# Optimization experiments

Hardware: AMD Instinct MI355X
Metric: run time of the kernel (lower is better)

The kernel has to match this reference:

```python
import jax, jax.numpy as jnp
import numpy as np

N_NODES = 50000
N_EDGES = 800000
HIDDEN = 128


def setup_inputs() -> dict:
    key = jax.random.key(0)
    k_h, k_src, k_dst, k_w1, k_w2 = jax.random.split(key, 5)
    h = jax.random.normal(k_h, (N_NODES, HIDDEN), dtype=jnp.float32)
    src = jax.random.randint(k_src, (N_EDGES,), 0, N_NODES, dtype=jnp.int32)
    dst = jax.random.randint(k_dst, (N_EDGES,), 0, N_NODES, dtype=jnp.int32)
    edge_index = jnp.stack([src, dst], axis=0)
    # MLP params (torch Linear: y = x @ W.T + b); store as [in, out] for einsum
    s1 = 1.0 / np.sqrt(2 * HIDDEN)
    s2 = 1.0 / np.sqrt(HIDDEN)
    W1 = jax.random.uniform(k_w1, (2 * HIDDEN, HIDDEN), jnp.float32, -s1, s1)
    b1 = jnp.zeros((HIDDEN,), jnp.float32)
    W2 = jax.random.uniform(k_w2, (HIDDEN, HIDDEN), jnp.float32, -s2, s2)
    b2 = jnp.zeros((HIDDEN,), jnp.float32)
    return {"h": h, "edge_index": edge_index, "W1": W1, "b1": b1, "W2": W2, "b2": b2}


def reference(h, edge_index, W1, b1, W2, b2):
    src, dst = edge_index[0], edge_index[1]
    n = h.shape[0]
    # scatter-add of gathered source features -> agg [N, H]
    agg = jax.ops.segment_sum(h[src], dst, num_segments=n)
    # degree normalization (clamp_min 1)
    deg = jax.ops.segment_sum(jnp.ones_like(dst, dtype=h.dtype), dst, num_segments=n)
    deg = jnp.maximum(deg, 1.0)[:, None]
    agg = agg / deg
    x = jnp.concatenate([h, agg], axis=1)  # [N, 2H]
    x = jax.nn.relu(x @ W1 + b1)
    x = jax.nn.relu(x @ W2 + b2)
    return x
```

## Files before the change

kernel.cpp:

```cpp
#include <hip/hip_runtime.h>

typedef unsigned short u16;
typedef unsigned int u32;
typedef __attribute__((ext_vector_type(8))) short short8;
typedef __attribute__((ext_vector_type(4))) float f32x4;
typedef __attribute__((ext_vector_type(4))) u32 u32x4;

#define BKT_SHIFT 7
#define BKT_NODES 128
#define CAP 3072
#define EPB 4096

__device__ inline u16 f2bf(float f){ u32 u=__float_as_uint(f); u32 r=((u>>16)&1u)+0x7fffu; return (u16)((u+r)>>16); }

__global__ __launch_bounds__(256) void k_cast(
    const float* __restrict__ h, u32* __restrict__ outw, int nh8,
    const float* __restrict__ w1, const float* __restrict__ w2,
    u16* __restrict__ w1t, u16* __restrict__ w2t,
    int* __restrict__ gcnt, int nbuck){
  int e = blockIdx.x*256 + threadIdx.x;
  if (e < nh8){
    float4 a = *(const float4*)(h + (size_t)e*8);
    float4 b = *(const float4*)(h + (size_t)e*8 + 4);
    u32x4 p;
    p.x = (u32)f2bf(a.x) | ((u32)f2bf(a.y)<<16);
    p.y = (u32)f2bf(a.z) | ((u32)f2bf(a.w)<<16);
    p.z = (u32)f2bf(b.x) | ((u32)f2bf(b.y)<<16);
    p.w = (u32)f2bf(b.z) | ((u32)f2bf(b.w)<<16);
    int node = e>>4, c8 = e&15;
    *(u32x4*)(outw + (size_t)node*128 + c8*4) = p;
  }
  if (e < 256*128){ int k=e>>7, nn=e&127; w1t[nn*256+k]=f2bf(w1[e]); }
  else { int j=e-256*128; if (j<128*128){ int k=j>>7, nn=j&127; w2t[nn*128+k]=f2bf(w2[j]); } }
  if (e < nbuck) gcnt[e] = 0;
}

__global__ __launch_bounds__(256) void k_bin(
    const int* __restrict__ src, const int* __restrict__ dst,
    int* __restrict__ gcnt, u32* __restrict__ recs_g, int nE){
  __shared__ u32 rl[EPB];
  __shared__ int hist[512];
  __shared__ int curs[512];
  int t = threadIdx.x;
  int e0 = blockIdx.x*EPB;
  for (int i=t;i<512;i+=256) hist[i]=0;
  __syncthreads();
  #pragma unroll
  for (int i=0;i<EPB/256;i++){
    int e = e0 + i*256 + t;
    u32 rec = 0xffffffffu;
    if (e < nE){
      u32 d = (u32)dst[e];
      u32 s = (u32)src[e];
      u32 b = d >> BKT_SHIFT;
      rec = (b<<23) | ((d & (u32)(BKT_NODES-1))<<16) | s;
      atomicAdd(&hist[b], 1);
    }
    rl[i*256+t] = rec;
  }
  __syncthreads();
  for (int i=t;i<512;i+=256){
    int c = hist[i];
    curs[i] = c ? atomicAdd(&gcnt[i], c) : 0;
  }
  __syncthreads();
  #pragma unroll
  for (int i=0;i<EPB/256;i++){
    u32 rec = rl[i*256+t];
    if (rec != 0xffffffffu){
      u32 b = rec>>23;
      int slot = atomicAdd(&curs[b], 1);
      if (slot < CAP) recs_g[(size_t)b*CAP + slot] = rec & 0x7fffffu;
    }
  }
}

__global__ __launch_bounds__(512) void k_agg2(
    const u32* __restrict__ recs_g, const int* __restrict__ gcnt,
    u32* __restrict__ outw, int n){
  __shared__ u32 stage[CAP];
  __shared__ u16 srt[CAP];
  __shared__ int hist[BKT_NODES];
  __shared__ int scn[BKT_NODES];
  __shared__ int cur[BKT_NODES];
  int b = blockIdx.x, t = threadIdx.x;
  int cnt = gcnt[b]; if (cnt > CAP) cnt = CAP;
  if (t < BKT_NODES) hist[t] = 0;
  __syncthreads();
  for (int i=t; i<cnt; i+=512){
    u32 r = recs_g[(size_t)b*CAP + i];
    stage[i] = r;
    atomicAdd(&hist[(r>>16)&(BKT_NODES-1)], 1);
  }
  __syncthreads();
  if (t < BKT_NODES) scn[t] = hist[t];
  __syncthreads();
  #pragma unroll
  for (int d=1; d<BKT_NODES; d<<=1){
    int v = 0;
    if (t < BKT_NODES){ v = scn[t]; if (t >= d) v += scn[t-d]; }
    __syncthreads();
    if (t < BKT_NODES) scn[t] = v;
    __syncthreads();
  }
  if (t < BKT_NODES) cur[t] = scn[t] - hist[t];
  __syncthreads();
  for (int i=t; i<cnt; i+=512){
    u32 r = stage[i];
    int slot = atomicAdd(&cur[(r>>16)&(BKT_NODES-1)], 1);
    srt[slot] = (u16)(r & 0xffffu);
  }
  __syncthreads();
  int wave = t>>6, lane = t&63;
  for (int nl=wave; nl<BKT_NODES; nl+=8){
    int node = b*BKT_NODES + nl;
    if (node >= n) continue;
    int deg = hist[nl];
    int st  = scn[nl] - deg;
    float a0=0.f, a1=0.f;
    int nfull = deg >> 4;
    for (int bb=0; bb<nfull; bb++){
      int base = st + bb*16;
      int sidx[16];
      #pragma unroll
      for (int j=0;j<16;j++) sidx[j] = srt[base+j];
      u32 vv[16];
      #pragma unroll
      for (int j=0;j<16;j++) vv[j] = outw[(size_t)sidx[j]*128 + lane];
      #pragma unroll
      for (int j=0;j<16;j++){
        union{u32 u; float f;} lo,hi; lo.u=vv[j]<<16; hi.u=vv[j]&0xffff0000u;
        a0 += lo.f; a1 += hi.f;
      }
    }
    int rem = deg & 15;
    if (rem){
      int base = st + nfull*16;
      int sidx[16];
      #pragma unroll
      for (int j=0;j<16;j++) sidx[j] = srt[base + (j<rem ? j : rem-1)];
      u32 vv[16];
      #pragma unroll
      for (int j=0;j<16;j++) vv[j] = outw[(size_t)sidx[j]*128 + lane];
      #pragma unroll
      for (int j=0;j<16;j++){
        float m = (j<rem) ? 1.f : 0.f;
        union{u32 u; float f;} lo,hi; lo.u=vv[j]<<16; hi.u=vv[j]&0xffff0000u;
        a0 += m*lo.f; a1 += m*hi.f;
      }
    }
    float inv = 1.f/(float)(deg>0?deg:1);
    outw[(size_t)node*128 + 64 + lane] = (u32)f2bf(a0*inv) | ((u32)f2bf(a1*inv)<<16);
  }
}

__global__ __launch_bounds__(256, 4) void k_mlp(
    const u32* __restrict__ outw_in,
    const u16* __restrict__ w1t, const u16* __restrict__ w2t,
    const float* __restrict__ b1, const float* __restrict__ b2,
    float* __restrict__ out, int n){
  __shared__ __align__(16) u16 xs[64*264];
  int t = threadIdx.x;
  int node0 = blockIdx.x*64;
  int wave=t>>6, lane=t&63, quad=lane>>4, l16=lane&15;
  int nt0 = wave*2;

  const u16* w1p0 = w1t + (size_t)((nt0  )*16 + l16)*256 + quad*8;
  const u16* w1p1 = w1t + (size_t)((nt0+1)*16 + l16)*256 + quad*8;
  short8 wb1[16];
  #pragma unroll
  for (int ks=0;ks<8;ks++){
    wb1[ks*2+0] = *(const short8*)(w1p0 + ks*32);
    wb1[ks*2+1] = *(const short8*)(w1p1 + ks*32);
  }

  #pragma unroll
  for (int i=0;i<8;i++){
    int idx = i*256 + t;
    int row = idx>>5, c8 = idx&31;
    int node = node0 + row;
    u32x4 v = {0,0,0,0};
    if (node < n) v = *(const u32x4*)(outw_in + (size_t)node*128 + c8*4);
    *(u32x4*)(&xs[row*264 + c8*8]) = v;
  }
  __syncthreads();

  f32x4 acc[4][2];
  #pragma unroll
  for (int m=0;m<4;m++){ acc[m][0]=(f32x4){0,0,0,0}; acc[m][1]=(f32x4){0,0,0,0}; }
  #pragma unroll
  for (int ks=0;ks<8;ks++){
    #pragma unroll
    for (int m=0;m<4;m++){
      short8 a = *(const short8*)(&xs[(m*16+l16)*264 + ks*32 + quad*8]);
      acc[m][0] = __builtin_amdgcn_mfma_f32_16x16x32_bf16(a, wb1[ks*2+0], acc[m][0],0,0,0);
      acc[m][1] = __builtin_amdgcn_mfma_f32_16x16x32_bf16(a, wb1[ks*2+1], acc[m][1],0,0,0);
    }
  }

  const u16* w2p0 = w2t + (size_t)((nt0  )*16 + l16)*128 + quad*8;
  const u16* w2p1 = w2t + (size_t)((nt0+1)*16 + l16)*128 + quad*8;
  short8 wb2[8];
  #pragma unroll
  for (int ks=0;ks<4;ks++){
    wb2[ks*2+0] = *(const short8*)(w2p0 + ks*32);
    wb2[ks*2+1] = *(const short8*)(w2p1 + ks*32);
  }

  __syncthreads();

  float bias0 = b1[(nt0  )*16 + l16];
  float bias1 = b1[(nt0+1)*16 + l16];
  #pragma unroll
  for (int m=0;m<4;m++){
    #pragma unroll
    for (int r=0;r<4;r++){
      int row = m*16 + quad*4 + r;
      float v0 = acc[m][0][r] + bias0; v0 = v0>0.f ? v0 : 0.f;
      float v1 = acc[m][1][r] + bias1; v1 = v1>0.f ? v1 : 0.f;
      xs[row*264 + (nt0  )*16 + l16] = f2bf(v0);
      xs[row*264 + (nt0+1)*16 + l16] = f2bf(v1);
    }
  }
  __syncthreads();

  f32x4 acc2[4][2];
  #pragma unroll
  for (int m=0;m<4;m++){ acc2[m][0]=(f32x4){0,0,0,0}; acc2[m][1]=(f32x4){0,0,0,0}; }
  #pragma unroll
  for (int ks=0;ks<4;ks++){
    #pragma unroll
    for (int m=0;m<4;m++){
      short8 a = *(const short8*)(&xs[(m*16+l16)*264 + ks*32 + quad*8]);
      acc2[m][0] = __builtin_amdgcn_mfma_f32_16x16x32_bf16(a, wb2[ks*2+0], acc2[m][0],0,0,0);
      acc2[m][1] = __builtin_amdgcn_mfma_f32_16x16x32_bf16(a, wb2[ks*2+1], acc2[m][1],0,0,0);
    }
  }
  float c0 = b2[(nt0  )*16 + l16];
  float c1 = b2[(nt0+1)*16 + l16];
  #pragma unroll
  for (int m=0;m<4;m++){
    #pragma unroll
    for (int r=0;r<4;r++){
      int node = node0 + m*16 + quad*4 + r;
      if (node<n){
        float v0 = acc2[m][0][r]+c0; v0 = v0>0.f?v0:0.f;
        float v1 = acc2[m][1][r]+c1; v1 = v1>0.f?v1:0.f;
        out[(size_t)node*128 + (nt0  )*16 + l16] = v0;
        out[(size_t)node*128 + (nt0+1)*16 + l16] = v1;
      }
    }
  }
}

extern "C" void kernel_launch(void* const* d_in, const int* in_sizes, int n_in,
                              void* d_out, int out_size, void* d_ws, size_t ws_size,
                              hipStream_t stream){
  const float* h  = (const float*)d_in[0];
  const int*   ei = (const int*)d_in[1];
  const float* W1 = (const float*)d_in[2];
  const float* b1 = (const float*)d_in[3];
  const float* W2 = (const float*)d_in[4];
  const float* b2 = (const float*)d_in[5];
  float* out = (float*)d_out;
  u32* outw  = (u32*)d_out;
  int n  = in_sizes[0] / 128;
  int nE = in_sizes[1] / 2;
  const int* srcI = ei;
  const int* dstI = ei + nE;
  int nbuck = (n + BKT_NODES - 1) >> BKT_SHIFT;

  char* ws = (char*)d_ws;
  u32* recs = (u32*)ws;
  size_t off = (size_t)nbuck*CAP*4;
  int* gcnt = (int*)(ws + off);
  off += (size_t)nbuck*4; off = (off + 15) & ~(size_t)15;
  u16* w1t = (u16*)(ws + off);
  u16* w2t = (u16*)(ws + off + 65536);

  int nh8 = n*16;
  int castN = nh8 > 49152 ? nh8 : 49152;
  k_cast<<<(castN+255)/256, 256, 0, stream>>>(h, outw, nh8, W1, W2, w1t, w2t, gcnt, nbuck);
  k_bin <<<(nE+EPB-1)/EPB, 256, 0, stream>>>(srcI, dstI, gcnt, recs, nE);
  k_agg2<<<nbuck, 512, 0, stream>>>(recs, gcnt, outw, n);
  k_mlp <<<(n+63)/64, 256, 0, stream>>>(outw, w1t, w2t, b1, b2, out, n);
}
```

Before: 157.1 us.

## Fuse cast with binning and aggregation with MLP into two kernels

Merges the bf16 cast and edge binning into one launch using disjoint block ranges. It also fuses the per-bucket aggregation with the two-layer MLP, so the aggregated features go straight to shared memory instead of a global round trip. Buckets shrink to 64 nodes to match the MLP tile, and the gather now uses 16-lane groups with 16-byte loads per node. A separate memset replaces the in-kernel counter clear. The tradeoffs are more shared memory and lower occupancy per block in the fused kernel, plus a smaller per-bucket capacity (1536) that could overflow on skewed inputs.

```diff
diff --git a/kernel.cpp b/kernel.cpp
--- a/kernel.cpp
+++ b/kernel.cpp
@@ -6,173 +6,87 @@
 typedef __attribute__((ext_vector_type(4))) float f32x4;
 typedef __attribute__((ext_vector_type(4))) u32 u32x4;
 
-#define BKT_SHIFT 7
-#define BKT_NODES 128
-#define CAP 3072
+#define BKT_SHIFT 6
+#define BKT_NODES 64
+#define CAP 1536
 #define EPB 4096
+#define NBH 1024
 
 __device__ inline u16 f2bf(float f){ u32 u=__float_as_uint(f); u32 r=((u>>16)&1u)+0x7fffu; return (u16)((u+r)>>16); }
 
-__global__ __launch_bounds__(256) void k_cast(
-    const float* __restrict__ h, u32* __restrict__ outw, int nh8,
+__global__ __launch_bounds__(256) void k_castbin(
+    const int* __restrict__ src, const int* __restrict__ dst,
+    int* __restrict__ gcnt, u32* __restrict__ recs_g, int nE, int gB,
+    const float* __restrict__ h, u16* __restrict__ hbf, int nh8,
     const float* __restrict__ w1, const float* __restrict__ w2,
-    u16* __restrict__ w1t, u16* __restrict__ w2t,
-    int* __restrict__ gcnt, int nbuck){
-  int e = blockIdx.x*256 + threadIdx.x;
-  if (e < nh8){
-    float4 a = *(const float4*)(h + (size_t)e*8);
-    float4 b = *(const float4*)(h + (size_t)e*8 + 4);
-    u32x4 p;
-    p.x = (u32)f2bf(a.x) | ((u32)f2bf(a.y)<<16);
-    p.y = (u32)f2bf(a.z) | ((u32)f2bf(a.w)<<16);
-    p.z = (u32)f2bf(b.x) | ((u32)f2bf(b.y)<<16);
-    p.w = (u32)f2bf(b.z) | ((u32)f2bf(b.w)<<16);
-    int node = e>>4, c8 = e&15;
-    *(u32x4*)(outw + (size_t)node*128 + c8*4) = p;
-  }
-  if (e < 256*128){ int k=e>>7, nn=e&127; w1t[nn*256+k]=f2bf(w1[e]); }
-  else { int j=e-256*128; if (j<128*128){ int k=j>>7, nn=j&127; w2t[nn*128+k]=f2bf(w2[j]); } }
-  if (e < nbuck) gcnt[e] = 0;
+    u16* __restrict__ w1t, u16* __restrict__ w2t){
+  __shared__ u32 rl[EPB];
+  __shared__ int hist[NBH];
+  __shared__ int curs[NBH];
+  int t = threadIdx.x;
+  if ((int)blockIdx.x < gB){
+    int e0 = blockIdx.x*EPB;
+    for (int i=t;i<NBH;i+=256) hist[i]=0;
+    __syncthreads();
+    #pragma unroll
+    for (int i=0;i<EPB/256;i++){
+      int e = e0 + i*256 + t;
+      u32 rec = 0xffffffffu;
+      if (e < nE){
+        u32 d = (u32)dst[e];
+        u32 s = (u32)src[e];
+        u32 bb = d >> BKT_SHIFT;
+        rec = (bb<<22) | ((d & (u32)(BKT_NODES-1))<<16) | s;
+        atomicAdd(&hist[bb & (NBH-1)], 1);
+      }
+      rl[i*256+t] = rec;
+    }
+    __syncthreads();
+    for (int i=t;i<NBH;i+=256){
+      int c = hist[i];
+      curs[i] = c ? atomicAdd(&gcnt[i], c) : 0;
+    }
+    __syncthreads();
+    #pragma unroll
+    for (int i=0;i<EPB/256;i++){
+      u32 rec = rl[i*256+t];
+      if (rec != 0xffffffffu){
+        u32 bb = rec>>22;
+        int slot = atomicAdd(&curs[bb], 1);
+        if (slot < CAP) recs_g[(size_t)bb*CAP + slot] = rec & 0x3fffffu;
+      }
+    }
+  } else {
+    int e = ((int)blockIdx.x - gB)*256 + t;
+    if (e < nh8){
+      float4 a = *(const float4*)(h + (size_t)e*8);
+      float4 b = *(const float4*)(h + (size_t)e*8 + 4);
+      u32x4 p;
+      p.x = (u32)f2bf(a.x) | ((u32)f2bf(a.y)<<16);
+      p.y = (u32)f2bf(a.z) | ((u32)f2bf(a.w)<<16);
+      p.z = (u32)f2bf(b.x) | ((u32)f2bf(b.y)<<16);
+      p.w = (u32)f2bf(b.z) | ((u32)f2bf(b.w)<<16);
+      *(u32x4*)(hbf + (size_t)e*8) = p;
+    }
+    if (e < 256*128){ int k=e>>7, nn=e&127; w1t[nn*256+k]=f2bf(w1[e]); }
+    else { int j=e-256*128; if (j<128*128){ int k=j>>7, nn=j&127; w2t[nn*128+k]=f2bf(w2[j]); } }
+  }
 }
 
-__global__ __launch_bounds__(256) void k_bin(
-    const int* __restrict__ src, const int* __restrict__ dst,
-    int* __restrict__ gcnt, u32* __restrict__ recs_g, int nE){
-  __shared__ u32 rl[EPB];
-  __shared__ int hist[512];
-  __shared__ int curs[512];
-  int t = threadIdx.x;
-  int e0 = blockIdx.x*EPB;
-  for (int i=t;i<512;i+=256) hist[i]=0;
-  __syncthreads();
-  #pragma unroll
-  for (int i=0;i<EPB/256;i++){
-    int e = e0 + i*256 + t;
-    u32 rec = 0xffffffffu;
-    if (e < nE){
-      u32 d = (u32)dst[e];
-      u32 s = (u32)src[e];
-      u32 b = d >> BKT_SHIFT;
-      rec = (b<<23) | ((d & (u32)(BKT_NODES-1))<<16) | s;
-      atomicAdd(&hist[b], 1);
-    }
-    rl[i*256+t] = rec;
-  }
-  __syncthreads();
-  for (int i=t;i<512;i+=256){
-    int c = hist[i];
-    curs[i] = c ? atomicAdd(&gcnt[i], c) : 0;
-  }
-  __syncthreads();
-  #pragma unroll
-  for (int i=0;i<EPB/256;i++){
-    u32 rec = rl[i*256+t];
-    if (rec != 0xffffffffu){
-      u32 b = rec>>23;
-      int slot = atomicAdd(&curs[b], 1);
-      if (slot < CAP) recs_g[(size_t)b*CAP + slot] = rec & 0x7fffffu;
-    }
-  }
-}
-
-__global__ __launch_bounds__(512) void k_agg2(
-    const u32* __restrict__ recs_g, const int* __restrict__ gcnt,
-    u32* __restrict__ outw, int n){
+__global__ __launch_bounds__(256, 3) void k_aggmlp(
+    const u16* __restrict__ hbf, const u32* __restrict__ recs_g,
+    const int* __restrict__ gcnt,
+    const u16* __restrict__ w1t, const u16* __restrict__ w2t,
+    const float* __restrict__ b1, const float* __restrict__ b2,
+    float* __restrict__ out, int n){
+  __shared__ __align__(16) u16 xs[64*264];
   __shared__ u32 stage[CAP];
   __shared__ u16 srt[CAP];
   __shared__ int hist[BKT_NODES];
   __shared__ int scn[BKT_NODES];
   __shared__ int cur[BKT_NODES];
   int b = blockIdx.x, t = threadIdx.x;
-  int cnt = gcnt[b]; if (cnt > CAP) cnt = CAP;
-  if (t < BKT_NODES) hist[t] = 0;
-  __syncthreads();
-  for (int i=t; i<cnt; i+=512){
-    u32 r = recs_g[(size_t)b*CAP + i];
-    stage[i] = r;
-    atomicAdd(&hist[(r>>16)&(BKT_NODES-1)], 1);
-  }
-  __syncthreads();
-  if (t < BKT_NODES) scn[t] = hist[t];
-  __syncthreads();
-  #pragma unroll
-  for (int d=1; d<BKT_NODES; d<<=1){
-    int v = 0;
-    if (t < BKT_NODES){ v = scn[t]; if (t >= d) v += scn[t-d]; }
-    __syncthreads();
-    if (t < BKT_NODES) scn[t] = v;
-    __syncthreads();
-  }
-  if (t < BKT_NODES) cur[t] = scn[t] - hist[t];
-  __syncthreads();
-  for (int i=t; i<cnt; i+=512){
-    u32 r = stage[i];
-    int slot = atomicAdd(&cur[(r>>16)&(BKT_NODES-1)], 1);
-    srt[slot] = (u16)(r & 0xffffu);
-  }
-  __syncthreads();
-  int wave = t>>6, lane = t&63;
-  for (int nl=wave; nl<BKT_NODES; nl+=8){
-    int node = b*BKT_NODES + nl;
-    if (node >= n) continue;
-    int deg = hist[nl];
-    int st  = scn[nl] - deg;
-    float a0=0.f, a1=0.f;
-    int nfull = deg >> 4;
-    for (int bb=0; bb<nfull; bb++){
-      int base = st + bb*16;
-      int sidx[16];
-      #pragma unroll
-      for (int j=0;j<16;j++) sidx[j] = srt[base+j];
-      u32 vv[16];
-      #pragma unroll
-      for (int j=0;j<16;j++) vv[j] = outw[(size_t)sidx[j]*128 + lane];
-      #pragma unroll
-      for (int j=0;j<16;j++){
-        union{u32 u; float f;} lo,hi; lo.u=vv[j]<<16; hi.u=vv[j]&0xffff0000u;
-        a0 += lo.f; a1 += hi.f;
-      }
-    }
-    int rem = deg & 15;
-    if (rem){
-      int base = st + nfull*16;
-      int sidx[16];
-      #pragma unroll
-      for (int j=0;j<16;j++) sidx[j] = srt[base + (j<rem ? j : rem-1)];
-      u32 vv[16];
-      #pragma unroll
-      for (int j=0;j<16;j++) vv[j] = outw[(size_t)sidx[j]*128 + lane];
-      #pragma unroll
-      for (int j=0;j<16;j++){
-        float m = (j<rem) ? 1.f : 0.f;
-        union{u32 u; float f;} lo,hi; lo.u=vv[j]<<16; hi.u=vv[j]&0xffff0000u;
-        a0 += m*lo.f; a1 += m*hi.f;
-      }
-    }
-    float inv = 1.f/(float)(deg>0?deg:1);
-    outw[(size_t)node*128 + 64 + lane] = (u32)f2bf(a0*inv) | ((u32)f2bf(a1*inv)<<16);
-  }
-}
-
-__global__ __launch_bounds__(256, 4) void k_mlp(
-    const u32* __restrict__ outw_in,
-    const u16* __restrict__ w1t, const u16* __restrict__ w2t,
-    const float* __restrict__ b1, const float* __restrict__ b2,
-    float* __restrict__ out, int n){
-  __shared__ __align__(16) u16 xs[64*264];
-  int t = threadIdx.x;
-  int node0 = blockIdx.x*64;
-  int wave=t>>6, lane=t&63, quad=lane>>4, l16=lane&15;
-  int nt0 = wave*2;
-
-  const u16* w1p0 = w1t + (size_t)((nt0  )*16 + l16)*256 + quad*8;
-  const u16* w1p1 = w1t + (size_t)((nt0+1)*16 + l16)*256 + quad*8;
-  short8 wb1[16];
-  #pragma unroll
-  for (int ks=0;ks<8;ks++){
-    wb1[ks*2+0] = *(const short8*)(w1p0 + ks*32);
-    wb1[ks*2+1] = *(const short8*)(w1p1 + ks*32);
-  }
+  int node0 = b*BKT_NODES;
 
   #pragma unroll
   for (int i=0;i<8;i++){
@@ -180,9 +94,89 @@
     int row = idx>>5, c8 = idx&31;
     int node = node0 + row;
     u32x4 v = {0,0,0,0};
-    if (node < n) v = *(const u32x4*)(outw_in + (size_t)node*128 + c8*4);
+    if (node < n && c8 < 16) v = *(const u32x4*)(hbf + (size_t)node*128 + c8*8);
     *(u32x4*)(&xs[row*264 + c8*8]) = v;
   }
+
+  int cnt = gcnt[b]; if (cnt > CAP) cnt = CAP;
+  if (t < BKT_NODES) hist[t] = 0;
+  __syncthreads();
+  for (int i=t; i<cnt; i+=256){
+    u32 r = recs_g[(size_t)b*CAP + i];
+    stage[i] = r;
+    atomicAdd(&hist[(r>>16)&(BKT_NODES-1)], 1);
+  }
+  __syncthreads();
+  if (t < BKT_NODES) scn[t] = hist[t];
+  __syncthreads();
+  #pragma unroll
+  for (int d=1; d<BKT_NODES; d<<=1){
+    int v = 0;
+    if (t < BKT_NODES){ v = scn[t]; if (t >= d) v += scn[t-d]; }
+    __syncthreads();
+    if (t < BKT_NODES) scn[t] = v;
+    __syncthreads();
+  }
+  if (t < BKT_NODES) cur[t] = scn[t] - hist[t];
+  __syncthreads();
+  for (int i=t; i<cnt; i+=256){
+    u32 r = stage[i];
+    int slot = atomicAdd(&cur[(r>>16)&(BKT_NODES-1)], 1);
+    srt[slot] = (u16)(r & 0xffffu);
+  }
+  __syncthreads();
+
+  int grp = t>>4, l16g = t&15;
+  for (int i=0;i<4;i++){
+    int nl = grp*4 + i;
+    int node = node0 + nl;
+    int deg = 0, st = 0;
+    if (node < n){ deg = hist[nl]; st = scn[nl] - deg; }
+    float a[8] = {0.f,0.f,0.f,0.f,0.f,0.f,0.f,0.f};
+    for (int base=0; base<deg; base+=16){
+      int sidx[16];
+      #pragma unroll
+      for (int j=0;j<16;j++){
+        int jj = base + j; if (jj > deg-1) jj = deg-1;
+        sidx[j] = srt[st + jj];
+      }
+      u32x4 vv[16];
+      #pragma unroll
+      for (int j=0;j<16;j++)
+        vv[j] = *(const u32x4*)(hbf + (size_t)sidx[j]*128 + l16g*8);
+      #pragma unroll
+      for (int j=0;j<16;j++){
+        float m = (base+j < deg) ? 1.f : 0.f;
+        #pragma unroll
+        for (int q=0;q<4;q++){
+          u32 u = vv[j][q];
+          union{u32 v; float f;} lo,hi; lo.v=u<<16; hi.v=u&0xffff0000u;
+          a[q*2]   += m*lo.f;
+          a[q*2+1] += m*hi.f;
+        }
+      }
+    }
+    if (node < n){
+      float inv = 1.f/(float)(deg>0?deg:1);
+      u32x4 o;
+      o.x = (u32)f2bf(a[0]*inv) | ((u32)f2bf(a[1]*inv)<<16);
+      o.y = (u32)f2bf(a[2]*inv) | ((u32)f2bf(a[3]*inv)<<16);
+      o.z = (u32)f2bf(a[4]*inv) | ((u32)f2bf(a[5]*inv)<<16);
+      o.w = (u32)f2bf(a[6]*inv) | ((u32)f2bf(a[7]*inv)<<16);
+      *(u32x4*)(&xs[nl*264 + 128 + l16g*8]) = o;
+    }
+  }
+
+  int wave=t>>6, lane=t&63, quad=lane>>4, l16=lane&15;
+  int nt0 = wave*2;
+  const u16* w1p0 = w1t + (size_t)((nt0  )*16 + l16)*256 + quad*8;
+  const u16* w1p1 = w1t + (size_t)((nt0+1)*16 + l16)*256 + quad*8;
+  short8 wb1[16];
+  #pragma unroll
+  for (int ks=0;ks<8;ks++){
+    wb1[ks*2+0] = *(const short8*)(w1p0 + ks*32);
+    wb1[ks*2+1] = *(const short8*)(w1p1 + ks*32);
+  }
   __syncthreads();
 
   f32x4 acc[4][2];
@@ -192,9 +186,9 @@
   for (int ks=0;ks<8;ks++){
     #pragma unroll
     for (int m=0;m<4;m++){
-      short8 a = *(const short8*)(&xs[(m*16+l16)*264 + ks*32 + quad*8]);
-      acc[m][0] = __builtin_amdgcn_mfma_f32_16x16x32_bf16(a, wb1[ks*2+0], acc[m][0],0,0,0);
-      acc[m][1] = __builtin_amdgcn_mfma_f32_16x16x32_bf16(a, wb1[ks*2+1], acc[m][1],0,0,0);
+      short8 av = *(const short8*)(&xs[(m*16+l16)*264 + ks*32 + quad*8]);
+      acc[m][0] = __builtin_amdgcn_mfma_f32_16x16x32_bf16(av, wb1[ks*2+0], acc[m][0],0,0,0);
+      acc[m][1] = __builtin_amdgcn_mfma_f32_16x16x32_bf16(av, wb1[ks*2+1], acc[m][1],0,0,0);
     }
   }
 
@@ -206,7 +200,6 @@
     wb2[ks*2+0] = *(const short8*)(w2p0 + ks*32);
     wb2[ks*2+1] = *(const short8*)(w2p1 + ks*32);
   }
-
   __syncthreads();
 
   float bias0 = b1[(nt0  )*16 + l16];
@@ -231,9 +224,9 @@
   for (int ks=0;ks<4;ks++){
     #pragma unroll
     for (int m=0;m<4;m++){
-      short8 a = *(const short8*)(&xs[(m*16+l16)*264 + ks*32 + quad*8]);
-      acc2[m][0] = __builtin_amdgcn_mfma_f32_16x16x32_bf16(a, wb2[ks*2+0], acc2[m][0],0,0,0);
-      acc2[m][1] = __builtin_amdgcn_mfma_f32_16x16x32_bf16(a, wb2[ks*2+1], acc2[m][1],0,0,0);
+      short8 av = *(const short8*)(&xs[(m*16+l16)*264 + ks*32 + quad*8]);
+      acc2[m][0] = __builtin_amdgcn_mfma_f32_16x16x32_bf16(av, wb2[ks*2+0], acc2[m][0],0,0,0);
+      acc2[m][1] = __builtin_amdgcn_mfma_f32_16x16x32_bf16(av, wb2[ks*2+1], acc2[m][1],0,0,0);
     }
   }
   float c0 = b2[(nt0  )*16 + l16];
@@ -263,7 +256,6 @@
   const float* W2 = (const float*)d_in[4];
   const float* b2 = (const float*)d_in[5];
   float* out = (float*)d_out;
-  u32* outw  = (u32*)d_out;
   int n  = in_sizes[0] / 128;
   int nE = in_sizes[1] / 2;
   const int* srcI = ei;
@@ -273,15 +265,18 @@
   char* ws = (char*)d_ws;
   u32* recs = (u32*)ws;
   size_t off = (size_t)nbuck*CAP*4;
-  int* gcnt = (int*)(ws + off);
-  off += (size_t)nbuck*4; off = (off + 15) & ~(size_t)15;
-  u16* w1t = (u16*)(ws + off);
-  u16* w2t = (u16*)(ws + off + 65536);
-
+  int* gcnt = (int*)(ws + off); off += 4096;
+  u16* hbf  = (u16*)(ws + off); off += (size_t)n*256;
+  off = (off + 15) & ~(size_t)15;
+  u16* w1t  = (u16*)(ws + off);
+  u16* w2t  = (u16*)(ws + off + 65536);
+
+  hipMemsetAsync(gcnt, 0, NBH*sizeof(int), stream);
+  int gB = (nE + EPB - 1)/EPB;
   int nh8 = n*16;
   int castN = nh8 > 49152 ? nh8 : 49152;
-  k_cast<<<(castN+255)/256, 256, 0, stream>>>(h, outw, nh8, W1, W2, w1t, w2t, gcnt, nbuck);
-  k_bin <<<(nE+EPB-1)/EPB, 256, 0, stream>>>(srcI, dstI, gcnt, recs, nE);
-  k_agg2<<<nbuck, 512, 0, stream>>>(recs, gcnt, outw, n);
-  k_mlp <<<(n+63)/64, 256, 0, stream>>>(outw, w1t, w2t, b1, b2, out, n);
+  int gC = (castN + 255)/256;
+  k_castbin<<<gB+gC, 256, 0, stream>>>(srcI, dstI, gcnt, recs, nE, gB,
+                                       h, hbf, nh8, W1, W2, w1t, w2t);
+  k_aggmlp<<<nbuck, 256, 0, stream>>>(hbf, recs, gcnt, w1t, w2t, b1, b2, out, n);
 }
```

Result: faster. 151.4 us (-3.6%).
